# Performance work log

Hardware: AMD Instinct MI355X
Metric: run time of the kernel (lower is better)

## Reference

```python
import jax, jax.numpy as jnp
import numpy as np

WINDOW_SIZE = 11
SIGMA = 1.5
NUM_CHANNEL = 1
C1 = 0.01 ** 2
C2 = 0.03 ** 2


def _gaussian_window(window_size: int, sigma: float, num_channel: int) -> jnp.ndarray:
    x = np.arange(window_size, dtype=np.float32)
    g = np.exp(-((x - window_size // 2) ** 2) / (2.0 * sigma ** 2))
    g = g / g.sum()
    w2d = np.outer(g, g).astype(np.float32)  # [K, K]
    # OIHW depthwise kernel: [C, 1, K, K]
    return jnp.asarray(np.broadcast_to(w2d, (num_channel, 1, window_size, window_size)).copy())


def _dwconv(x: jnp.ndarray, window: jnp.ndarray) -> jnp.ndarray:
    k = window.shape[-1]
    pad = k // 2
    return jax.lax.conv_general_dilated(
        x, window,
        window_strides=(1, 1),
        padding=[(pad, pad), (pad, pad)],
        dimension_numbers=("NCHW", "OIHW", "NCHW"),
        feature_group_count=x.shape[1],
    )


def setup_inputs() -> dict:
    key = jax.random.key(0)
    k1, k2 = jax.random.split(key)
    shape = (32, 1, 512, 512)
    X_gt = jax.random.uniform(k1, shape, dtype=jnp.float32)
    X_pred = jax.random.uniform(k2, shape, dtype=jnp.float32)
    return {"X_gt": X_gt, "X_pred": X_pred}


def reference(X_gt, X_pred):
    window = _gaussian_window(WINDOW_SIZE, SIGMA, X_gt.shape[1]).astype(X_gt.dtype)
    mu1 = _dwconv(X_gt, window)
    mu2 = _dwconv(X_pred, window)
    sq_mu1 = mu1 * mu1
    sq_mu2 = mu2 * mu2
    sigma1 = _dwconv(X_gt * X_gt, window) - sq_mu1
    sigma2 = _dwconv(X_pred * X_pred, window) - sq_mu2
    sigma = _dwconv(X_gt * X_pred, window) - mu1 * mu2
    ssim_map = ((2.0 * (mu1 * mu2) + C1) * (2.0 * sigma + C2)) / (
        (sq_mu1 + sq_mu2 + C1) * (sq_mu1 + sq_mu2 + C2)
    )
    # size_average=True -> scalar mean
    return ssim_map.mean()
```

## Files before the change

kernel.cpp:

```cpp
#include <hip/hip_runtime.h>
#include <math.h>

#define IMG_H 512
#define IMG_W 512
#define KW 11
#define RAD 5
#define T 8
#define NG (IMG_W / 4)

#define C1F (0.01f * 0.01f)
#define C2F (0.03f * 0.03f)

__device__ __forceinline__ float ssim_px(float mu1, float mu2, float sp) {
    float m12 = mu1 * mu2;
    float sigma = sp - m12;
    float sq = mu1 * mu1 + mu2 * mu2;
    return ((2.f * m12 + C1F) * (2.f * sigma + C2F)) / ((sq + C1F) * (sq + C2F));
}

__global__ __launch_bounds__(256, 2)
void ssim_fused_kernel(const float* __restrict__ A, const float* __restrict__ B,
                       float* __restrict__ out, float inv_total) {
    __shared__ float wpart[4];

    const int tid = threadIdx.x;
    const int g = tid & (NG - 1);
    const int rchunk = tid >> 7;
    const int img = blockIdx.y;
    const int ybase = blockIdx.x * (2 * T) + rchunk * T;

    float w[KW];
    {
        float s = 0.f;
#pragma unroll
        for (int i = 0; i < KW; ++i) {
            float d = (float)(i - RAD);
            w[i] = expf(-(d * d) / 4.5f);
            s += w[i];
        }
        float inv = 1.0f / s;
#pragma unroll
        for (int i = 0; i < KW; ++i) {
            w[i] *= inv;
            w[i] = __int_as_float(__builtin_amdgcn_readfirstlane(__float_as_int(w[i])));
        }
    }

    const float* __restrict__ Ai = A + (size_t)img * IMG_H * IMG_W;
    const float* __restrict__ Bi = B + (size_t)img * IMG_H * IMG_W;

    float4 accA[T], accB[T], accP[T];
#pragma unroll
    for (int o = 0; o < T; ++o) {
        accA[o] = make_float4(0.f, 0.f, 0.f, 0.f);
        accB[o] = accA[o];
        accP[o] = accA[o];
    }

#pragma unroll
    for (int i = 0; i < T + 2 * RAD; ++i) {
        int gy = ybase + i - RAD;
        if (gy >= 0 && gy < IMG_H) {
            const float* rowA = Ai + (size_t)gy * IMG_W;
            const float* rowB = Bi + (size_t)gy * IMG_W;

            float fa[20], fb[20];
#pragma unroll
            for (int m = 0; m < 5; ++m) {
                int gm = g + m - 2;
                float4 va = make_float4(0.f, 0.f, 0.f, 0.f);
                float4 vb = va;
                if ((unsigned)gm < (unsigned)NG) {
                    va = *(const float4*)(rowA + 4 * gm);
                    vb = *(const float4*)(rowB + 4 * gm);
                }
                fa[4 * m] = va.x; fa[4 * m + 1] = va.y; fa[4 * m + 2] = va.z; fa[4 * m + 3] = va.w;
                fb[4 * m] = vb.x; fb[4 * m + 1] = vb.y; fb[4 * m + 2] = vb.z; fb[4 * m + 3] = vb.w;
            }

            float4 hA = make_float4(0.f, 0.f, 0.f, 0.f);
            float4 hB = hA, hP = hA;
#pragma unroll
            for (int k = 0; k < KW; ++k) {
                float wk = w[k];
                hA.x += wk * fa[3 + k];  hA.y += wk * fa[4 + k];
                hA.z += wk * fa[5 + k];  hA.w += wk * fa[6 + k];
                hB.x += wk * fb[3 + k];  hB.y += wk * fb[4 + k];
                hB.z += wk * fb[5 + k];  hB.w += wk * fb[6 + k];
                hP.x += wk * (fa[3 + k] * fb[3 + k]);
                hP.y += wk * (fa[4 + k] * fb[4 + k]);
                hP.z += wk * (fa[5 + k] * fb[5 + k]);
                hP.w += wk * (fa[6 + k] * fb[6 + k]);
            }

#pragma unroll
            for (int o = 0; o < T; ++o) {
                if (i - o >= 0 && i - o < KW) {
                    float wk = w[i - o];
                    accA[o].x += wk * hA.x; accA[o].y += wk * hA.y;
                    accA[o].z += wk * hA.z; accA[o].w += wk * hA.w;
                    accB[o].x += wk * hB.x; accB[o].y += wk * hB.y;
                    accB[o].z += wk * hB.z; accB[o].w += wk * hB.w;
                    accP[o].x += wk * hP.x; accP[o].y += wk * hP.y;
                    accP[o].z += wk * hP.z; accP[o].w += wk * hP.w;
                }
            }
        }
    }

    float acc = 0.f;
#pragma unroll
    for (int o = 0; o < T; ++o) {
        acc += ssim_px(accA[o].x, accB[o].x, accP[o].x);
        acc += ssim_px(accA[o].y, accB[o].y, accP[o].y);
        acc += ssim_px(accA[o].z, accB[o].z, accP[o].z);
        acc += ssim_px(accA[o].w, accB[o].w, accP[o].w);
    }

#pragma unroll
    for (int off = 32; off > 0; off >>= 1)
        acc += __shfl_down(acc, off, 64);
    int wid = tid >> 6;
    int lane = tid & 63;
    if (lane == 0) wpart[wid] = acc;
    __syncthreads();
    if (tid == 0) {
        float s = (wpart[0] + wpart[1]) + (wpart[2] + wpart[3]);
        atomicAdd(out, s * inv_total);
    }
}

extern "C" void kernel_launch(void* const* d_in, const int* in_sizes, int n_in,
                              void* d_out, int out_size, void* d_ws, size_t ws_size,
                              hipStream_t stream) {
    const float* A = (const float*)d_in[0];
    const float* B = (const float*)d_in[1];
    float* out = (float*)d_out;

    const int total = in_sizes[0];
    const int nimg = total / (IMG_H * IMG_W);

    hipMemsetAsync(d_out, 0, sizeof(float), stream);

    dim3 grid(IMG_H / (2 * T), nimg, 1);
    ssim_fused_kernel<<<grid, 256, 0, stream>>>(A, B, out, 1.0f / (float)total);
}
```

Before: 142.3 us.

## Shrink row tile and halo loads to raise occupancy

Halves the per-thread output rows from 8 to 4 and raises the launch-bounds occupancy hint from 2 to 5 blocks per CU. The horizontal halo load drops from five float4s to three float4s plus two scalar loads, cutting per-row loads and register footprint. The products a*b are precomputed once per loaded element instead of inside the tap loop. The trade-off is that vertical halo overhead grows (14 rows loaded for 4 outputs instead of 18 for 8), which increases redundant global and L2 traffic in exchange for more waves in flight.

After: 336.4 us. 137% more time.

```diff
diff --git a/kernel.cpp b/kernel.cpp
--- a/kernel.cpp
+++ b/kernel.cpp
@@ -5,7 +5,7 @@
 #define IMG_W 512
 #define KW 11
 #define RAD 5
-#define T 8
+#define T 4
 #define NG (IMG_W / 4)
 
 #define C1F (0.01f * 0.01f)
@@ -18,7 +18,7 @@
     return ((2.f * m12 + C1F) * (2.f * sigma + C2F)) / ((sq + C1F) * (sq + C2F));
 }
 
-__global__ __launch_bounds__(256, 2)
+__global__ __launch_bounds__(256, 5)
 void ssim_fused_kernel(const float* __restrict__ A, const float* __restrict__ B,
                        float* __restrict__ out, float inv_total) {
     __shared__ float wpart[4];
@@ -64,33 +64,61 @@
             const float* rowA = Ai + (size_t)gy * IMG_W;
             const float* rowB = Bi + (size_t)gy * IMG_W;
 
-            float fa[20], fb[20];
-#pragma unroll
-            for (int m = 0; m < 5; ++m) {
-                int gm = g + m - 2;
+            float fa[14], fb[14];
+            {
+                int c = 4 * g - 5;
+                bool v = (c >= 0);
+                fa[0] = v ? rowA[c] : 0.f;
+                fb[0] = v ? rowB[c] : 0.f;
+            }
+            {
                 float4 va = make_float4(0.f, 0.f, 0.f, 0.f);
                 float4 vb = va;
-                if ((unsigned)gm < (unsigned)NG) {
-                    va = *(const float4*)(rowA + 4 * gm);
-                    vb = *(const float4*)(rowB + 4 * gm);
+                if (g >= 1) {
+                    va = *(const float4*)(rowA + 4 * (g - 1));
+                    vb = *(const float4*)(rowB + 4 * (g - 1));
                 }
-                fa[4 * m] = va.x; fa[4 * m + 1] = va.y; fa[4 * m + 2] = va.z; fa[4 * m + 3] = va.w;
-                fb[4 * m] = vb.x; fb[4 * m + 1] = vb.y; fb[4 * m + 2] = vb.z; fb[4 * m + 3] = vb.w;
+                fa[1] = va.x; fa[2] = va.y; fa[3] = va.z; fa[4] = va.w;
+                fb[1] = vb.x; fb[2] = vb.y; fb[3] = vb.z; fb[4] = vb.w;
             }
+            {
+                float4 va = *(const float4*)(rowA + 4 * g);
+                float4 vb = *(const float4*)(rowB + 4 * g);
+                fa[5] = va.x; fa[6] = va.y; fa[7] = va.z; fa[8] = va.w;
+                fb[5] = vb.x; fb[6] = vb.y; fb[7] = vb.z; fb[8] = vb.w;
+            }
+            {
+                float4 va = make_float4(0.f, 0.f, 0.f, 0.f);
+                float4 vb = va;
+                if (g <= NG - 2) {
+                    va = *(const float4*)(rowA + 4 * (g + 1));
+                    vb = *(const float4*)(rowB + 4 * (g + 1));
+                }
+                fa[9]  = va.x; fa[10] = va.y; fa[11] = va.z; fa[12] = va.w;
+                fb[9]  = vb.x; fb[10] = vb.y; fb[11] = vb.z; fb[12] = vb.w;
+            }
+            {
+                int c = 4 * g + 8;
+                bool v = (c < IMG_W);
+                fa[13] = v ? rowA[c] : 0.f;
+                fb[13] = v ? rowB[c] : 0.f;
+            }
+
+            float p[14];
+#pragma unroll
+            for (int j = 0; j < 14; ++j) p[j] = fa[j] * fb[j];
 
             float4 hA = make_float4(0.f, 0.f, 0.f, 0.f);
             float4 hB = hA, hP = hA;
 #pragma unroll
             for (int k = 0; k < KW; ++k) {
                 float wk = w[k];
-                hA.x += wk * fa[3 + k];  hA.y += wk * fa[4 + k];
-                hA.z += wk * fa[5 + k];  hA.w += wk * fa[6 + k];
-                hB.x += wk * fb[3 + k];  hB.y += wk * fb[4 + k];
-                hB.z += wk * fb[5 + k];  hB.w += wk * fb[6 + k];
-                hP.x += wk * (fa[3 + k] * fb[3 + k]);
-                hP.y += wk * (fa[4 + k] * fb[4 + k]);
-                hP.z += wk * (fa[5 + k] * fb[5 + k]);
-                hP.w += wk * (fa[6 + k] * fb[6 + k]);
+                hA.x += wk * fa[k];     hA.y += wk * fa[k + 1];
+                hA.z += wk * fa[k + 2]; hA.w += wk * fa[k + 3];
+                hB.x += wk * fb[k];     hB.y += wk * fb[k + 1];
+                hB.z += wk * fb[k + 2]; hB.w += wk * fb[k + 3];
+                hP.x += wk * p[k];      hP.y += wk * p[k + 1];
+                hP.z += wk * p[k + 2];  hP.w += wk * p[k + 3];
             }
 
 #pragma unroll
```

## Software-pipeline row loads with double buffering, halve row tile, raise occupancy

Applied to the files above, without the earlier changes.

Each thread now loads the next input row into registers while it computes the current one, alternating between two register buffer sets. The horizontal window is built from three float4 loads plus two scalar edge loads per image instead of five float4 loads. Output rows per thread drop from 8 to 4 and the launch bound is raised to allow four blocks per CU, aiming to hide memory latency through occupancy and prefetch. In exchange, halo overhead grows: 14 input rows are processed per 4 outputs instead of 18 per 8, which adds redundant horizontal filtering and global loads per output.

After: 461.4 us. +224.4%, slower.

```diff
diff --git a/kernel.cpp b/kernel.cpp
--- a/kernel.cpp
+++ b/kernel.cpp
@@ -5,7 +5,8 @@
 #define IMG_W 512
 #define KW 11
 #define RAD 5
-#define T 8
+#define T 4
+#define NROWS (T + 2 * RAD)
 #define NG (IMG_W / 4)
 
 #define C1F (0.01f * 0.01f)
@@ -18,7 +19,7 @@
     return ((2.f * m12 + C1F) * (2.f * sigma + C2F)) / ((sq + C1F) * (sq + C2F));
 }
 
-__global__ __launch_bounds__(256, 2)
+__global__ __launch_bounds__(256, 4)
 void ssim_fused_kernel(const float* __restrict__ A, const float* __restrict__ B,
                        float* __restrict__ out, float inv_total) {
     __shared__ float wpart[4];
@@ -57,56 +58,108 @@
         accP[o] = accA[o];
     }
 
-#pragma unroll
-    for (int i = 0; i < T + 2 * RAD; ++i) {
-        int gy = ybase + i - RAD;
-        if (gy >= 0 && gy < IMG_H) {
-            const float* rowA = Ai + (size_t)gy * IMG_W;
-            const float* rowB = Bi + (size_t)gy * IMG_W;
-
-            float fa[20], fb[20];
-#pragma unroll
-            for (int m = 0; m < 5; ++m) {
-                int gm = g + m - 2;
-                float4 va = make_float4(0.f, 0.f, 0.f, 0.f);
-                float4 vb = va;
-                if ((unsigned)gm < (unsigned)NG) {
-                    va = *(const float4*)(rowA + 4 * gm);
-                    vb = *(const float4*)(rowB + 4 * gm);
-                }
-                fa[4 * m] = va.x; fa[4 * m + 1] = va.y; fa[4 * m + 2] = va.z; fa[4 * m + 3] = va.w;
-                fb[4 * m] = vb.x; fb[4 * m + 1] = vb.y; fb[4 * m + 2] = vb.z; fb[4 * m + 3] = vb.w;
-            }
-
-            float4 hA = make_float4(0.f, 0.f, 0.f, 0.f);
-            float4 hB = hA, hP = hA;
-#pragma unroll
-            for (int k = 0; k < KW; ++k) {
-                float wk = w[k];
-                hA.x += wk * fa[3 + k];  hA.y += wk * fa[4 + k];
-                hA.z += wk * fa[5 + k];  hA.w += wk * fa[6 + k];
-                hB.x += wk * fb[3 + k];  hB.y += wk * fb[4 + k];
-                hB.z += wk * fb[5 + k];  hB.w += wk * fb[6 + k];
-                hP.x += wk * (fa[3 + k] * fb[3 + k]);
-                hP.y += wk * (fa[4 + k] * fb[4 + k]);
-                hP.z += wk * (fa[5 + k] * fb[5 + k]);
-                hP.w += wk * (fa[6 + k] * fb[6 + k]);
-            }
-
-#pragma unroll
-            for (int o = 0; o < T; ++o) {
-                if (i - o >= 0 && i - o < KW) {
-                    float wk = w[i - o];
-                    accA[o].x += wk * hA.x; accA[o].y += wk * hA.y;
-                    accA[o].z += wk * hA.z; accA[o].w += wk * hA.w;
-                    accB[o].x += wk * hB.x; accB[o].y += wk * hB.y;
-                    accB[o].z += wk * hB.z; accB[o].w += wk * hB.w;
-                    accP[o].x += wk * hP.x; accP[o].y += wk * hP.y;
-                    accP[o].z += wk * hP.z; accP[o].w += wk * hP.w;
-                }
-            }
-        }
-    }
+    const float4 z4 = make_float4(0.f, 0.f, 0.f, 0.f);
+    float4 eA0 = z4, eA1 = z4, eA2 = z4, eB0 = z4, eB1 = z4, eB2 = z4;
+    float4 oA0 = z4, oA1 = z4, oA2 = z4, oB0 = z4, oB1 = z4, oB2 = z4;
+
+#define PRE(P, GY)                                                        \
+    {                                                                     \
+        int gy2_ = (GY);                                                  \
+        if (gy2_ >= 0 && gy2_ < IMG_H) {                                  \
+            const float* rA_ = Ai + (size_t)gy2_ * IMG_W;                 \
+            const float* rB_ = Bi + (size_t)gy2_ * IMG_W;                 \
+            if (g >= 1) {                                                 \
+                P##A0 = *(const float4*)(rA_ + 4 * (g - 1));              \
+                P##B0 = *(const float4*)(rB_ + 4 * (g - 1));              \
+            }                                                             \
+            P##A1 = *(const float4*)(rA_ + 4 * g);                        \
+            P##B1 = *(const float4*)(rB_ + 4 * g);                        \
+            if (g <= NG - 2) {                                            \
+                P##A2 = *(const float4*)(rA_ + 4 * (g + 1));              \
+                P##B2 = *(const float4*)(rB_ + 4 * (g + 1));              \
+            }                                                             \
+        }                                                                 \
+    }
+
+#define HJ(J)                                                             \
+    {                                                                     \
+        float t_ = fa[J] * fb[J];                                         \
+        _Pragma("unroll")                                                 \
+        for (int c_ = 0; c_ < 4; ++c_) {                                  \
+            int k_ = (J) - c_;                                            \
+            if (k_ >= 0 && k_ < KW) {                                     \
+                hA[c_] += w[k_] * fa[J];                                  \
+                hB[c_] += w[k_] * fb[J];                                  \
+                hP[c_] += w[k_] * t_;                                     \
+            }                                                             \
+        }                                                                 \
+    }
+
+#define CONS(I, P)                                                        \
+    {                                                                     \
+        int gy_ = ybase + (I) - RAD;                                      \
+        if (gy_ >= 0 && gy_ < IMG_H) {                                    \
+            const float* rA_ = Ai + (size_t)gy_ * IMG_W;                  \
+            const float* rB_ = Bi + (size_t)gy_ * IMG_W;                  \
+            int cl_ = 4 * g - 5, cr_ = 4 * g + 8;                         \
+            float ea0_ = (cl_ >= 0) ? rA_[cl_] : 0.f;                     \
+            float eb0_ = (cl_ >= 0) ? rB_[cl_] : 0.f;                     \
+            float ea1_ = (cr_ < IMG_W) ? rA_[cr_] : 0.f;                  \
+            float eb1_ = (cr_ < IMG_W) ? rB_[cr_] : 0.f;                  \
+            float fa[14] = {ea0_, P##A0.x, P##A0.y, P##A0.z, P##A0.w,     \
+                            P##A1.x, P##A1.y, P##A1.z, P##A1.w,           \
+                            P##A2.x, P##A2.y, P##A2.z, P##A2.w, ea1_};    \
+            float fb[14] = {eb0_, P##B0.x, P##B0.y, P##B0.z, P##B0.w,     \
+                            P##B1.x, P##B1.y, P##B1.z, P##B1.w,           \
+                            P##B2.x, P##B2.y, P##B2.z, P##B2.w, eb1_};    \
+            float hA[4] = {0.f, 0.f, 0.f, 0.f};                           \
+            float hB[4] = {0.f, 0.f, 0.f, 0.f};                           \
+            float hP[4] = {0.f, 0.f, 0.f, 0.f};                           \
+            HJ(0) HJ(1) HJ(2) HJ(3) HJ(4) HJ(5) HJ(6)                     \
+            HJ(7) HJ(8) HJ(9) HJ(10) HJ(11) HJ(12) HJ(13)                 \
+            _Pragma("unroll")                                             \
+            for (int o_ = 0; o_ < T; ++o_) {                              \
+                int k_ = (I) - o_;                                        \
+                if (k_ >= 0 && k_ < KW) {                                 \
+                    float wk_ = w[k_];                                    \
+                    accA[o_].x += wk_ * hA[0]; accA[o_].y += wk_ * hA[1]; \
+                    accA[o_].z += wk_ * hA[2]; accA[o_].w += wk_ * hA[3]; \
+                    accB[o_].x += wk_ * hB[0]; accB[o_].y += wk_ * hB[1]; \
+                    accB[o_].z += wk_ * hB[2]; accB[o_].w += wk_ * hB[3]; \
+                    accP[o_].x += wk_ * hP[0]; accP[o_].y += wk_ * hP[1]; \
+                    accP[o_].z += wk_ * hP[2]; accP[o_].w += wk_ * hP[3]; \
+                }                                                         \
+            }                                                             \
+        }                                                                 \
+    }
+
+#define STEP(I, CP, NP)                                                   \
+    {                                                                     \
+        if ((I) + 1 < NROWS) PRE(NP, ybase + (I) + 1 - RAD)               \
+        CONS(I, CP)                                                       \
+    }
+
+    PRE(e, ybase - RAD)
+
+    STEP(0, e, o)
+    STEP(1, o, e)
+    STEP(2, e, o)
+    STEP(3, o, e)
+    STEP(4, e, o)
+    STEP(5, o, e)
+    STEP(6, e, o)
+    STEP(7, o, e)
+    STEP(8, e, o)
+    STEP(9, o, e)
+    STEP(10, e, o)
+    STEP(11, o, e)
+    STEP(12, e, o)
+    STEP(13, o, e)
+
+#undef STEP
+#undef CONS
+#undef HJ
+#undef PRE
 
     float acc = 0.f;
 #pragma unroll
```

## Stage input rows through double-buffered LDS and shrink row tile

Applied to the files above, without the earlier changes.

Each thread now handles two columns and reads its horizontal neighbourhood from shared memory instead of issuing overlapping global float4 loads. Rows are loaded in phases of four into a double-buffered LDS ring, with the next phase's global loads issued before the current phase is consumed. The row tile drops from 8 to 4 and the grid doubles. Vertical halo overhead per output row rises from 10/8 to 10/4, so more rows are re-read, in exchange for fewer redundant horizontal loads and more blocks in flight.

Result: slower. 153.3 us (+7.8%).

```diff
diff --git a/kernel.cpp b/kernel.cpp
--- a/kernel.cpp
+++ b/kernel.cpp
@@ -5,8 +5,9 @@
 #define IMG_W 512
 #define KW 11
 #define RAD 5
-#define T 8
-#define NG (IMG_W / 4)
+#define T 4
+#define NROWS (T + 2 * RAD)
+#define LROW 548
 
 #define C1F (0.01f * 0.01f)
 #define C2F (0.03f * 0.03f)
@@ -21,13 +22,14 @@
 __global__ __launch_bounds__(256, 2)
 void ssim_fused_kernel(const float* __restrict__ A, const float* __restrict__ B,
                        float* __restrict__ out, float inv_total) {
+    __shared__ float sA[2][4][LROW];
+    __shared__ float sB[2][4][LROW];
     __shared__ float wpart[4];
 
     const int tid = threadIdx.x;
-    const int g = tid & (NG - 1);
-    const int rchunk = tid >> 7;
+    const int c0 = 2 * tid;
     const int img = blockIdx.y;
-    const int ybase = blockIdx.x * (2 * T) + rchunk * T;
+    const int ybase = blockIdx.x * T;
 
     float w[KW];
     {
@@ -49,72 +51,117 @@
     const float* __restrict__ Ai = A + (size_t)img * IMG_H * IMG_W;
     const float* __restrict__ Bi = B + (size_t)img * IMG_H * IMG_W;
 
-    float4 accA[T], accB[T], accP[T];
+    float aA0[T], aA1[T], aB0[T], aB1[T], aP0[T], aP1[T];
 #pragma unroll
     for (int o = 0; o < T; ++o) {
-        accA[o] = make_float4(0.f, 0.f, 0.f, 0.f);
-        accB[o] = accA[o];
-        accP[o] = accA[o];
+        aA0[o] = 0.f; aA1[o] = 0.f;
+        aB0[o] = 0.f; aB1[o] = 0.f;
+        aP0[o] = 0.f; aP1[o] = 0.f;
     }
 
+    if (tid < 8) {
 #pragma unroll
-    for (int i = 0; i < T + 2 * RAD; ++i) {
-        int gy = ybase + i - RAD;
-        if (gy >= 0 && gy < IMG_H) {
-            const float* rowA = Ai + (size_t)gy * IMG_W;
-            const float* rowB = Bi + (size_t)gy * IMG_W;
+        for (int b = 0; b < 2; ++b)
+#pragma unroll
+            for (int s = 0; s < 4; ++s) {
+                sA[b][s][tid] = 0.f;       sB[b][s][tid] = 0.f;
+                sA[b][s][520 + tid] = 0.f; sB[b][s][520 + tid] = 0.f;
+            }
+    }
 
-            float fa[20], fb[20];
-#pragma unroll
-            for (int m = 0; m < 5; ++m) {
-                int gm = g + m - 2;
-                float4 va = make_float4(0.f, 0.f, 0.f, 0.f);
-                float4 vb = va;
-                if ((unsigned)gm < (unsigned)NG) {
-                    va = *(const float4*)(rowA + 4 * gm);
-                    vb = *(const float4*)(rowB + 4 * gm);
-                }
-                fa[4 * m] = va.x; fa[4 * m + 1] = va.y; fa[4 * m + 2] = va.z; fa[4 * m + 3] = va.w;
-                fb[4 * m] = vb.x; fb[4 * m + 1] = vb.y; fb[4 * m + 2] = vb.z; fb[4 * m + 3] = vb.w;
-            }
+    float2 rgA[4], rgB[4];
 
-            float4 hA = make_float4(0.f, 0.f, 0.f, 0.f);
-            float4 hB = hA, hP = hA;
-#pragma unroll
-            for (int k = 0; k < KW; ++k) {
-                float wk = w[k];
-                hA.x += wk * fa[3 + k];  hA.y += wk * fa[4 + k];
-                hA.z += wk * fa[5 + k];  hA.w += wk * fa[6 + k];
-                hB.x += wk * fb[3 + k];  hB.y += wk * fb[4 + k];
-                hB.z += wk * fb[5 + k];  hB.w += wk * fb[6 + k];
-                hP.x += wk * (fa[3 + k] * fb[3 + k]);
-                hP.y += wk * (fa[4 + k] * fb[4 + k]);
-                hP.z += wk * (fa[5 + k] * fb[5 + k]);
-                hP.w += wk * (fa[6 + k] * fb[6 + k]);
-            }
+#define LOADPH(P, NS)                                                     \
+    {                                                                     \
+        _Pragma("unroll")                                                 \
+        for (int s_ = 0; s_ < (NS); ++s_) {                               \
+            int gy_ = ybase - RAD + 4 * (P) + s_;                         \
+            float2 a_ = make_float2(0.f, 0.f);                            \
+            float2 b_ = make_float2(0.f, 0.f);                            \
+            if (gy_ >= 0 && gy_ < IMG_H) {                                \
+                a_ = *(const float2*)(Ai + (size_t)gy_ * IMG_W + c0);     \
+                b_ = *(const float2*)(Bi + (size_t)gy_ * IMG_W + c0);     \
+            }                                                             \
+            rgA[s_] = a_; rgB[s_] = b_;                                   \
+        }                                                                 \
+    }
 
-#pragma unroll
-            for (int o = 0; o < T; ++o) {
-                if (i - o >= 0 && i - o < KW) {
-                    float wk = w[i - o];
-                    accA[o].x += wk * hA.x; accA[o].y += wk * hA.y;
-                    accA[o].z += wk * hA.z; accA[o].w += wk * hA.w;
-                    accB[o].x += wk * hB.x; accB[o].y += wk * hB.y;
-                    accB[o].z += wk * hB.z; accB[o].w += wk * hB.w;
-                    accP[o].x += wk * hP.x; accP[o].y += wk * hP.y;
-                    accP[o].z += wk * hP.z; accP[o].w += wk * hP.w;
-                }
-            }
-        }
+#define WRITEPH(BUF, NS)                                                  \
+    {                                                                     \
+        _Pragma("unroll")                                                 \
+        for (int s_ = 0; s_ < (NS); ++s_) {                               \
+            *(float2*)&sA[BUF][s_][c0 + 8] = rgA[s_];                     \
+            *(float2*)&sB[BUF][s_][c0 + 8] = rgB[s_];                     \
+        }                                                                 \
     }
+
+#define CONSROW(BUF, S, I)                                                \
+    {                                                                     \
+        float2 qa[7], qb[7];                                              \
+        _Pragma("unroll")                                                 \
+        for (int j_ = 0; j_ < 7; ++j_) {                                  \
+            qa[j_] = *(const float2*)&sA[BUF][S][c0 + 2 + 2 * j_];        \
+            qb[j_] = *(const float2*)&sB[BUF][S][c0 + 2 + 2 * j_];        \
+        }                                                                 \
+        float fa[14] = {qa[0].x, qa[0].y, qa[1].x, qa[1].y, qa[2].x,      \
+                        qa[2].y, qa[3].x, qa[3].y, qa[4].x, qa[4].y,      \
+                        qa[5].x, qa[5].y, qa[6].x, qa[6].y};              \
+        float fb[14] = {qb[0].x, qb[0].y, qb[1].x, qb[1].y, qb[2].x,      \
+                        qb[2].y, qb[3].x, qb[3].y, qb[4].x, qb[4].y,      \
+                        qb[5].x, qb[5].y, qb[6].x, qb[6].y};              \
+        float p[14];                                                      \
+        _Pragma("unroll")                                                 \
+        for (int m_ = 1; m_ < 13; ++m_) p[m_] = fa[m_] * fb[m_];          \
+        float h0A = 0.f, h1A = 0.f, h0B = 0.f, h1B = 0.f;                 \
+        float h0P = 0.f, h1P = 0.f;                                       \
+        _Pragma("unroll")                                                 \
+        for (int k_ = 0; k_ < KW; ++k_) {                                 \
+            float wk_ = w[k_];                                            \
+            h0A += wk_ * fa[k_ + 1]; h1A += wk_ * fa[k_ + 2];             \
+            h0B += wk_ * fb[k_ + 1]; h1B += wk_ * fb[k_ + 2];             \
+            h0P += wk_ * p[k_ + 1];  h1P += wk_ * p[k_ + 2];              \
+        }                                                                 \
+        _Pragma("unroll")                                                 \
+        for (int o_ = 0; o_ < T; ++o_) {                                  \
+            int k_ = (I) - o_;                                            \
+            if (k_ >= 0 && k_ < KW) {                                     \
+                float wk_ = w[k_];                                        \
+                aA0[o_] += wk_ * h0A; aA1[o_] += wk_ * h1A;               \
+                aB0[o_] += wk_ * h0B; aB1[o_] += wk_ * h1B;               \
+                aP0[o_] += wk_ * h0P; aP1[o_] += wk_ * h1P;               \
+            }                                                             \
+        }                                                                 \
+    }
+
+    LOADPH(0, 4) WRITEPH(0, 4)
+    __syncthreads();
+
+    LOADPH(1, 4)
+    CONSROW(0, 0, 0) CONSROW(0, 1, 1) CONSROW(0, 2, 2) CONSROW(0, 3, 3)
+    WRITEPH(1, 4)
+    __syncthreads();
+
+    LOADPH(2, 4)
+    CONSROW(1, 0, 4) CONSROW(1, 1, 5) CONSROW(1, 2, 6) CONSROW(1, 3, 7)
+    WRITEPH(0, 4)
+    __syncthreads();
+
+    LOADPH(3, 2)
+    CONSROW(0, 0, 8) CONSROW(0, 1, 9) CONSROW(0, 2, 10) CONSROW(0, 3, 11)
+    WRITEPH(1, 2)
+    __syncthreads();
+
+    CONSROW(1, 0, 12) CONSROW(1, 1, 13)
+
+#undef CONSROW
+#undef WRITEPH
+#undef LOADPH
 
     float acc = 0.f;
 #pragma unroll
     for (int o = 0; o < T; ++o) {
-        acc += ssim_px(accA[o].x, accB[o].x, accP[o].x);
-        acc += ssim_px(accA[o].y, accB[o].y, accP[o].y);
-        acc += ssim_px(accA[o].z, accB[o].z, accP[o].z);
-        acc += ssim_px(accA[o].w, accB[o].w, accP[o].w);
+        acc += ssim_px(aA0[o], aB0[o], aP0[o]);
+        acc += ssim_px(aA1[o], aB1[o], aP1[o]);
     }
 
 #pragma unroll
@@ -142,6 +189,6 @@
 
     hipMemsetAsync(d_out, 0, sizeof(float), stream);
 
-    dim3 grid(IMG_H / (2 * T), nimg, 1);
+    dim3 grid(IMG_H / T, nimg, 1);
     ssim_fused_kernel<<<grid, 256, 0, stream>>>(A, B, out, 1.0f / (float)total);
 }
```
